# Kernel optimization log

Hardware: AMD Instinct MI355X
Metric: run time of the kernel (lower is better)

The kernel has to match this reference:

```python
import jax, jax.numpy as jnp
import numpy as np
import math

DIM = 1024
H = 16
DK = DIM // H
SEG = 512
NN = 2      # num_neighbors
DIL = 4     # dilation
B, L = 2, 8192


def setup_inputs() -> dict:
    key = jax.random.key(0)
    ks = jax.random.split(key, 9)
    scale = 1.0 / math.sqrt(DIM)
    def lin(k):
        return jax.random.normal(k, (DIM, DIM), jnp.float32) * scale
    return {
        "x": jax.random.normal(ks[0], (B, L, DIM), jnp.float32),
        "Wq": lin(ks[1]), "bq": jnp.zeros((DIM,), jnp.float32),
        "Wk": lin(ks[2]), "bk": jnp.zeros((DIM,), jnp.float32),
        "Wv": lin(ks[3]), "bv": jnp.zeros((DIM,), jnp.float32),
        "Wo": lin(ks[4]), "bo": jnp.zeros((DIM,), jnp.float32),
    }


def _attn(q, k, v):
    # q: [B,S,H,Q,dk], k/v: [B,S,H,K,dk]
    scores = jnp.einsum('bshqd,bshkd->bshqk', q, k) / math.sqrt(q.shape[-1])
    a = jax.nn.softmax(scores, axis=-1)
    return jnp.einsum('bshqk,bshkd->bshqd', a, v)


def reference(x, Wq, bq, Wk, bk, Wv, bv, Wo, bo):
    Bx, Lx, C = x.shape
    pad = (-Lx) % SEG

    def proj_chunk(W, b):
        t = x @ W + b                                  # [B,L,C]
        t = jnp.pad(t, ((0, 0), (0, pad), (0, 0)))
        S = t.shape[1] // SEG
        t = t.reshape(Bx, S, SEG, H, DK)
        return t.transpose(0, 1, 3, 2, 4)              # [B,S,H,seg,dk]

    q = proj_chunk(Wq, bq)
    k = proj_chunk(Wk, bk)
    v = proj_chunk(Wv, bv)
    S = q.shape[1]

    # segment-local dense attention (vectorized over all segments)
    out = _attn(q, k, v)

    # dilated sampling of neighbor segments' keys/values
    dil_idx = jnp.arange(0, SEG, DIL)
    kd = k[:, :, :, dil_idx, :]                        # [B,S,H,seg/DIL,dk]
    vd = v[:, :, :, dil_idx, :]

    seg_ids = jnp.arange(S)
    w = 1.0 / (2 * NN)
    for off in range(1, NN + 1):
        for sign in (-1, 1):
            n = seg_ids + sign * off
            valid = (n >= 0) & (n < S)                 # [S]
            nc = jnp.clip(n, 0, S - 1)
            cross = _attn(q, kd[:, nc], vd[:, nc])     # [B,S,H,seg,dk]
            out = out + jnp.where(valid[None, :, None, None, None], cross * w, 0.0)

    out = out.transpose(0, 1, 3, 2, 4).reshape(Bx, S * SEG, C)
    out = out[:, :Lx, :]
    return out @ Wo + bo
```

## Files before the change

### kernel.cpp

```cpp
#include <hip/hip_runtime.h>
#include <stdint.h>

typedef __attribute__((ext_vector_type(8))) short short8;
typedef __attribute__((ext_vector_type(4))) float f32x4;

#define MFMA16(A_, B_, C_) __builtin_amdgcn_mfma_f32_16x16x32_bf16((A_), (B_), (C_), 0, 0, 0)

#if __has_builtin(__builtin_amdgcn_exp2f)
#define EXP2(x) __builtin_amdgcn_exp2f(x)
#else
#define EXP2(x) exp2f(x)
#endif

#define GLDS16(g_, l_)                                                        \
  __builtin_amdgcn_global_load_lds(                                           \
      (const __attribute__((address_space(1))) void*)(g_),                    \
      (__attribute__((address_space(3))) void*)(l_), 16, 0, 0)

__device__ __forceinline__ unsigned short f2bf(float f) {
  unsigned int u = __float_as_uint(f);
  u += 0x7fffu + ((u >> 16) & 1u);
  return (unsigned short)(u >> 16);
}

__device__ __forceinline__ unsigned pk2(float a, float b) {
  return (__float_as_uint(a) >> 16) | (__float_as_uint(b) & 0xffff0000u);
}


__global__ void cast_x_kernel(const float* __restrict__ x,
                              unsigned short* __restrict__ xb, int n8) {
  int i = blockIdx.x * blockDim.x + threadIdx.x;
  if (i >= n8) return;
  const float4* x4 = reinterpret_cast<const float4*>(x);
  float4 a = x4[2 * i], b = x4[2 * i + 1];
  uint4 o;
  o.x = (unsigned)f2bf(a.x) | ((unsigned)f2bf(a.y) << 16);
  o.y = (unsigned)f2bf(a.z) | ((unsigned)f2bf(a.w) << 16);
  o.z = (unsigned)f2bf(b.x) | ((unsigned)f2bf(b.y) << 16);
  o.w = (unsigned)f2bf(b.z) | ((unsigned)f2bf(b.w) << 16);
  reinterpret_cast<uint4*>(xb)[i] = o;
}

__global__ void transpose_cast4_kernel(const float* __restrict__ W0,
                                       const float* __restrict__ W1,
                                       const float* __restrict__ W2,
                                       const float* __restrict__ W3,
                                       unsigned short* __restrict__ T0,
                                       unsigned short* __restrict__ T1,
                                       unsigned short* __restrict__ T2,
                                       unsigned short* __restrict__ T3) {
  __shared__ float tile[32][33];
  const float* W = (blockIdx.z == 0) ? W0 : (blockIdx.z == 1) ? W1
                   : (blockIdx.z == 2) ? W2 : W3;
  unsigned short* Wt = (blockIdx.z == 0) ? T0 : (blockIdx.z == 1) ? T1
                       : (blockIdx.z == 2) ? T2 : T3;
  int k0 = blockIdx.x * 32, n0 = blockIdx.y * 32;
  int tx = threadIdx.x, ty = threadIdx.y;
  for (int i = ty; i < 32; i += 8)
    tile[i][tx] = W[(size_t)(k0 + i) * 1024 + n0 + tx];
  __syncthreads();
  for (int i = ty; i < 32; i += 8)
    Wt[(size_t)(n0 + i) * 1024 + k0 + tx] = f2bf(tile[tx][i]);
}

template<int MODE>
__global__ __launch_bounds__(256, 2) void gemm_kernel(
    const unsigned short* __restrict__ A,
    const unsigned short* __restrict__ W,
    const float* __restrict__ bias,
    unsigned short* __restrict__ out_bf,
    unsigned short* __restrict__ out_vtd,
    float* __restrict__ out_f) {
  __shared__ unsigned short Asm[2][128 * 64];
  __shared__ unsigned short Bsm[2][128 * 64];
  const int t = threadIdx.x;
  const int wg = (blockIdx.x & 7) * 128 + (blockIdx.x >> 3);
  const int m0 = (wg >> 3) * 128;
  const int n0 = (wg & 7) * 128;
  const int w = t >> 6, lane = t & 63, lr = lane & 15, lg = lane >> 4;
  const int wm = w >> 1, wn = w & 1;

  f32x4 acc[4][4];
#pragma unroll
  for (int i = 0; i < 4; ++i)
#pragma unroll
    for (int j = 0; j < 4; ++j) acc[i][j] = f32x4{0.f, 0.f, 0.f, 0.f};

  const int srow = lane >> 3;
  const int sswz = ((lane & 7) ^ srow) * 8;
  const int mrow = m0 + w * 32 + srow;
  const unsigned short* gA;
  size_t astep, arstride;
  if (MODE == 3) {
    gA = A + (size_t)(mrow >> 9) * (16 * 32768) + (size_t)(mrow & 511) * 64 + sswz;
    astep = 32768;
    arstride = 8 * 64;
  } else {
    gA = A + (size_t)mrow * 1024 + sswz;
    astep = 64;
    arstride = 8 * 1024;
  }
  const unsigned short* gB = W + (size_t)(n0 + w * 32 + srow) * 1024 + sswz;

  auto stage = [&](int buf, int kt) {
    const unsigned short* ga = gA + (size_t)kt * astep;
    const unsigned short* gb = gB + (size_t)kt * 64;
    unsigned short* la = &Asm[buf][(w * 32) * 64];
    unsigned short* lb = &Bsm[buf][(w * 32) * 64];
#pragma unroll
    for (int p = 0; p < 4; ++p) {
      GLDS16(ga + (size_t)p * arstride, la + p * 8 * 64);
      GLDS16(gb + (size_t)(p * 8) * 1024, lb + p * 8 * 64);
    }
  };

  const int rswz = (lr & 7);
  auto compute = [&](int buf) {
    const unsigned short* bA = &Asm[buf][0];
    const unsigned short* bB = &Bsm[buf][0];
    short8 bfv[2][4];
#pragma unroll
    for (int ks = 0; ks < 2; ++ks)
#pragma unroll
      for (int j = 0; j < 4; ++j) {
        const int row = wn * 64 + j * 16 + lr;
        bfv[ks][j] = *reinterpret_cast<const short8*>(
            &bB[row * 64 + (((ks * 4 + lg) ^ rswz) * 8)]);
      }
#pragma unroll
    for (int i = 0; i < 4; ++i) {
      const int row = wm * 64 + i * 16 + lr;
      short8 af[2];
#pragma unroll
      for (int ks = 0; ks < 2; ++ks)
        af[ks] = *reinterpret_cast<const short8*>(
            &bA[row * 64 + (((ks * 4 + lg) ^ rswz) * 8)]);
#pragma unroll
      for (int ks = 0; ks < 2; ++ks)
#pragma unroll
        for (int j = 0; j < 4; ++j)
          acc[i][j] = MFMA16(af[ks], bfv[ks][j], acc[i][j]);
    }
  };

  stage(0, 0);
#pragma unroll 1
  for (int kt = 0; kt < 15; ++kt) {
    stage((kt + 1) & 1, kt + 1);
    asm volatile("s_waitcnt vmcnt(8)\n\ts_barrier" ::: "memory");
    compute(kt & 1);
    asm volatile("s_waitcnt lgkmcnt(0)\n\ts_barrier" ::: "memory");
  }
  asm volatile("s_waitcnt vmcnt(0)\n\ts_barrier" ::: "memory");
  compute(1);

#pragma unroll
  for (int i = 0; i < 4; ++i)
#pragma unroll
    for (int j = 0; j < 4; ++j) {
      const int n = n0 + wn * 64 + j * 16 + lr;
      const float bv = bias[n];
#pragma unroll
      for (int r = 0; r < 4; ++r) {
        const int m = m0 + wm * 64 + i * 16 + lg * 4 + r;
        float val = acc[i][j][r] + bv;
        if (MODE == 3) {
          out_f[(size_t)m * 1024 + n] = val;
        } else {
          const int b = m >> 13, ll = m & 8191;
          const int ss = ll >> 9, rr = ll & 511;
          const int hh = n >> 6, d = n & 63;
          const size_t head = (size_t)((b * 16 + ss) * 16 + hh);
          if (MODE == 0) {
            out_bf[head * 32768 + rr * 64 + d] = f2bf(val * 0.18033688011112042f);
          } else if (MODE == 1) {
            out_bf[head * 32768 + rr * 64 + d] = f2bf(val);
          } else {
            const int p32 = (((rr >> 2) & 3) << 3) | (((rr >> 4) & 1) << 2) | (rr & 3);
            out_bf[head * 32768 + (size_t)d * 512 + ((rr & ~31) | p32)] = f2bf(val);
            if ((rr & 3) == 0) {
              const int cd = rr >> 2;
              const int pd = (((cd >> 2) & 3) << 3) | (((cd >> 4) & 1) << 2) | (cd & 3);
              out_vtd[head * 8192 + (size_t)d * 128 + ((cd & ~31) | pd)] = f2bf(val);
            }
          }
        }
      }
    }
}

__device__ __forceinline__ void attn_group(
    const unsigned short* __restrict__ Kp, int kstride,
    const unsigned short* __restrict__ Vp, int vstride,
    int nchunks, float wgt,
    const short8 (&qf)[2][2],
    unsigned short* __restrict__ Kl, unsigned short* __restrict__ Vl,
    f32x4 (&total)[2][4],
    int lr, int lg, int w, int lane) {
  const int srow = lane >> 3;
  const int fcw = (lane & 7) ^ srow;
  const unsigned short* gK = Kp + (size_t)(w * 8 + srow) * kstride + fcw * 8;
  const unsigned short* gV = Vp + (size_t)(w * 8 + srow) * vstride + fcw * 8;
  const int sx = lr & 7;

  float l[2][2] = {{0.f, 0.f}, {0.f, 0.f}};
  f32x4 acc[2][4];
#pragma unroll
  for (int rt = 0; rt < 2; ++rt)
#pragma unroll
    for (int dt = 0; dt < 4; ++dt) acc[rt][dt] = f32x4{0.f, 0.f, 0.f, 0.f};

  GLDS16(gK, Kl + w * 512);
  GLDS16(gV, Vl + w * 512);
  __syncthreads();

  int cur = 0;
  for (int c = 0; c < nchunks; ++c) {
    if (c + 1 < nchunks) {
      GLDS16(gK + (size_t)((c + 1) * 64) * kstride, Kl + (cur ^ 1) * 4096 + w * 512);
      GLDS16(gV + (c + 1) * 64, Vl + (cur ^ 1) * 4096 + w * 512);
    }
    const unsigned short* bK = Kl + cur * 4096;
    const unsigned short* bV = Vl + cur * 4096;

    short8 pf[2][2];
#pragma unroll
    for (int kp = 0; kp < 2; ++kp) {
      f32x4 s0[2], s1[2];
#pragma unroll
      for (int rt = 0; rt < 2; ++rt) {
        s0[rt] = f32x4{0.f, 0.f, 0.f, 0.f};
        s1[rt] = f32x4{0.f, 0.f, 0.f, 0.f};
      }
      __builtin_amdgcn_s_setprio(1);
#pragma unroll
      for (int ks = 0; ks < 2; ++ks) {
        const int rc = (((ks * 4 + lg) ^ sx) * 8);
        short8 kf0 = *reinterpret_cast<const short8*>(&bK[(kp * 32 + lr) * 64 + rc]);
        short8 kf1 = *reinterpret_cast<const short8*>(&bK[(kp * 32 + 16 + lr) * 64 + rc]);
#pragma unroll
        for (int rt = 0; rt < 2; ++rt) {
          s0[rt] = MFMA16(kf0, qf[rt][ks], s0[rt]);
          s1[rt] = MFMA16(kf1, qf[rt][ks], s1[rt]);
        }
      }
      __builtin_amdgcn_s_setprio(0);
#pragma unroll
      for (int rt = 0; rt < 2; ++rt) {
        float e0 = EXP2(s0[rt][0]), e1 = EXP2(s0[rt][1]);
        float e2 = EXP2(s0[rt][2]), e3 = EXP2(s0[rt][3]);
        float e4 = EXP2(s1[rt][0]), e5 = EXP2(s1[rt][1]);
        float e6 = EXP2(s1[rt][2]), e7 = EXP2(s1[rt][3]);
        l[rt][kp] += ((e0 + e1) + (e2 + e3)) + ((e4 + e5) + (e6 + e7));
        uint4 wv;
        wv.x = pk2(e0, e1); wv.y = pk2(e2, e3);
        wv.z = pk2(e4, e5); wv.w = pk2(e6, e7);
        pf[rt][kp] = *reinterpret_cast<short8*>(&wv);
      }
    }
    __builtin_amdgcn_s_setprio(1);
#pragma unroll
    for (int ks = 0; ks < 2; ++ks) {
      const int rcv = (((ks * 4 + lg) ^ sx) * 8);
#pragma unroll
      for (int dt = 0; dt < 4; ++dt) {
        short8 vf = *reinterpret_cast<const short8*>(&bV[(dt * 16 + lr) * 64 + rcv]);
#pragma unroll
        for (int rt = 0; rt < 2; ++rt)
          acc[rt][dt] = MFMA16(pf[rt][ks], vf, acc[rt][dt]);
      }
    }
    __builtin_amdgcn_s_setprio(0);
    __syncthreads();
    cur ^= 1;
  }
#pragma unroll
  for (int rt = 0; rt < 2; ++rt) {
    float s = l[rt][0] + l[rt][1];
    s += __shfl_xor(s, 16);
    s += __shfl_xor(s, 32);
    float rl[4];
#pragma unroll
    for (int r = 0; r < 4; ++r) rl[r] = wgt / __shfl(s, lg * 4 + r);
#pragma unroll
    for (int dt = 0; dt < 4; ++dt)
#pragma unroll
      for (int r = 0; r < 4; ++r) total[rt][dt][r] += acc[rt][dt][r] * rl[r];
  }
}

__global__ __launch_bounds__(512) void attn_kernel(
    const unsigned short* __restrict__ Q,
    const unsigned short* __restrict__ K,
    const unsigned short* __restrict__ Vt,
    const unsigned short* __restrict__ Vtd,
    unsigned short* __restrict__ AO) {
  __shared__ unsigned short Kl[2 * 4096];
  __shared__ unsigned short Vl[2 * 4096];
  const int wg = blockIdx.x;
  const int qh = wg & 1;
  const int bsh = wg >> 1;
  const int h = bsh & 15, s = (bsh >> 4) & 15, b = bsh >> 8;
  const int t = threadIdx.x, w = t >> 6, lane = t & 63, lr = lane & 15, lg = lane >> 4;
  const int q0 = qh * 256 + w * 32;

  const size_t headbase = (size_t)((b * 16 + s) * 16 + h);
  const unsigned short* Qp = Q + headbase * 32768 + (size_t)q0 * 64;
  short8 qf[2][2];
#pragma unroll
  for (int rt = 0; rt < 2; ++rt)
#pragma unroll
    for (int ks = 0; ks < 2; ++ks)
      qf[rt][ks] = *reinterpret_cast<const short8*>(&Qp[(rt * 16 + lr) * 64 + ks * 32 + lg * 8]);

  f32x4 total[2][4];
#pragma unroll
  for (int rt = 0; rt < 2; ++rt)
#pragma unroll
    for (int dt = 0; dt < 4; ++dt) total[rt][dt] = f32x4{0.f, 0.f, 0.f, 0.f};

  attn_group(K + headbase * 32768, 64, Vt + headbase * 32768, 512, 8, 1.0f,
             qf, Kl, Vl, total, lr, lg, w, lane);
#pragma unroll
  for (int gi = 0; gi < 4; ++gi) {
    const int off = (gi == 0) ? -2 : (gi == 1) ? -1 : (gi == 2) ? 1 : 2;
    const int ns = s + off;
    if (ns < 0 || ns > 15) continue;
    const size_t hb = (size_t)((b * 16 + ns) * 16 + h);
    attn_group(K + hb * 32768, 256, Vtd + hb * 8192, 128, 2, 0.25f,
               qf, Kl, Vl, total, lr, lg, w, lane);
  }
  const size_t obase = headbase * 32768 + (size_t)q0 * 64;
#pragma unroll
  for (int rt = 0; rt < 2; ++rt)
#pragma unroll
    for (int dt = 0; dt < 4; ++dt)
#pragma unroll
      for (int r = 0; r < 4; ++r) {
        const int q = rt * 16 + lg * 4 + r;
        const int d = dt * 16 + lr;
        AO[obase + (size_t)q * 64 + d] = f2bf(total[rt][dt][r]);
      }
}

extern "C" void kernel_launch(void* const* d_in, const int* in_sizes, int n_in,
                              void* d_out, int out_size, void* d_ws, size_t ws_size,
                              hipStream_t stream) {
  const float* x  = (const float*)d_in[0];
  const float* Wq = (const float*)d_in[1];
  const float* bq = (const float*)d_in[2];
  const float* Wk = (const float*)d_in[3];
  const float* bk = (const float*)d_in[4];
  const float* Wv = (const float*)d_in[5];
  const float* bv = (const float*)d_in[6];
  const float* Wo = (const float*)d_in[7];
  const float* bo = (const float*)d_in[8];
  float* out = (float*)d_out;

  char* ws = (char*)d_ws;
  unsigned short* Xb   = (unsigned short*)(ws);
  unsigned short* Wqt  = (unsigned short*)(ws + 33554432);
  unsigned short* Wkt  = (unsigned short*)(ws + 35651584);
  unsigned short* Wvt  = (unsigned short*)(ws + 37748736);
  unsigned short* Wot  = (unsigned short*)(ws + 39845888);
  unsigned short* Qb   = (unsigned short*)(ws + 41943040);
  unsigned short* Kb   = (unsigned short*)(ws + 75497472);
  unsigned short* Vtb  = (unsigned short*)(ws + 109051904);
  unsigned short* Vtdb = (unsigned short*)(ws + 142606336);
  unsigned short* AOb  = (unsigned short*)(ws + 150994944);

  cast_x_kernel<<<8192, 256, 0, stream>>>(x, Xb, 2097152);
  dim3 tb(32, 8), tg(32, 32, 4);
  transpose_cast4_kernel<<<tg, tb, 0, stream>>>(Wq, Wk, Wv, Wo, Wqt, Wkt, Wvt, Wot);

  gemm_kernel<0><<<1024, 256, 0, stream>>>(Xb, Wqt, bq, Qb, nullptr, nullptr);
  gemm_kernel<1><<<1024, 256, 0, stream>>>(Xb, Wkt, bk, Kb, nullptr, nullptr);
  gemm_kernel<2><<<1024, 256, 0, stream>>>(Xb, Wvt, bv, Vtb, Vtdb, nullptr);

  attn_kernel<<<1024, 512, 0, stream>>>(Qb, Kb, Vtb, Vtdb, AOb);

  gemm_kernel<3><<<1024, 256, 0, stream>>>(AOb, Wot, bo, nullptr, nullptr, out);
}
```

Baseline: 292.1 us.

## Enlarge GEMM tiles to 256x256 with 32x32 MFMA and remap attention blocks

The projection and output GEMMs move from 128x128 tiles with 4 waves to 256x256 tiles with 8 waves per block. They now use 32x32x16 bf16 MFMA instructions in place of 16x16x32, with the fragment indexing and epilogue row mapping updated to match. The grid shrinks to 256 blocks, about one per CU, which is meant to raise operand reuse and cut LDS reads per MFMA. The cost is 128KB of LDS per block and a single wave of blocks that may leave little latency hiding. The attention kernel's block index is also reordered so the two query halves of a head land in different halves of the grid.

```diff
diff --git a/kernel.cpp b/kernel.cpp
--- a/kernel.cpp
+++ b/kernel.cpp
@@ -3,8 +3,10 @@
 
 typedef __attribute__((ext_vector_type(8))) short short8;
 typedef __attribute__((ext_vector_type(4))) float f32x4;
+typedef __attribute__((ext_vector_type(16))) float f32x16;
 
 #define MFMA16(A_, B_, C_) __builtin_amdgcn_mfma_f32_16x16x32_bf16((A_), (B_), (C_), 0, 0, 0)
+#define MFMA32(A_, B_, C_) __builtin_amdgcn_mfma_f32_32x32x16_bf16((A_), (B_), (C_), 0, 0, 0)
 
 #if __has_builtin(__builtin_amdgcn_exp2f)
 #define EXP2(x) __builtin_amdgcn_exp2f(x)
@@ -65,27 +67,30 @@
 }
 
 template<int MODE>
-__global__ __launch_bounds__(256, 2) void gemm_kernel(
+__global__ __launch_bounds__(512, 2) void gemm_kernel(
     const unsigned short* __restrict__ A,
     const unsigned short* __restrict__ W,
     const float* __restrict__ bias,
     unsigned short* __restrict__ out_bf,
     unsigned short* __restrict__ out_vtd,
     float* __restrict__ out_f) {
-  __shared__ unsigned short Asm[2][128 * 64];
-  __shared__ unsigned short Bsm[2][128 * 64];
+  __shared__ unsigned short Asm[2][256 * 64];
+  __shared__ unsigned short Bsm[2][256 * 64];
   const int t = threadIdx.x;
-  const int wg = (blockIdx.x & 7) * 128 + (blockIdx.x >> 3);
-  const int m0 = (wg >> 3) * 128;
-  const int n0 = (wg & 7) * 128;
-  const int w = t >> 6, lane = t & 63, lr = lane & 15, lg = lane >> 4;
-  const int wm = w >> 1, wn = w & 1;
-
-  f32x4 acc[4][4];
+  const int wg = (blockIdx.x & 7) * 32 + (blockIdx.x >> 3);
+  const int m0 = (wg >> 2) * 256;
+  const int n0 = (wg & 3) * 256;
+  const int w = t >> 6, lane = t & 63;
+  const int wm = w >> 2, wn = w & 3;
+  const int rl = lane & 31, l5 = lane >> 5;
+
+  f32x16 acc[4][2];
 #pragma unroll
   for (int i = 0; i < 4; ++i)
 #pragma unroll
-    for (int j = 0; j < 4; ++j) acc[i][j] = f32x4{0.f, 0.f, 0.f, 0.f};
+    for (int j = 0; j < 2; ++j)
+#pragma unroll
+      for (int e = 0; e < 16; ++e) acc[i][j][e] = 0.f;
 
   const int srow = lane >> 3;
   const int sswz = ((lane & 7) ^ srow) * 8;
@@ -115,32 +120,32 @@
     }
   };
 
-  const int rswz = (lr & 7);
+  const int rswz = (rl & 7);
   auto compute = [&](int buf) {
     const unsigned short* bA = &Asm[buf][0];
     const unsigned short* bB = &Bsm[buf][0];
-    short8 bfv[2][4];
-#pragma unroll
-    for (int ks = 0; ks < 2; ++ks)
-#pragma unroll
-      for (int j = 0; j < 4; ++j) {
-        const int row = wn * 64 + j * 16 + lr;
+    short8 bfv[4][2];
+#pragma unroll
+    for (int ks = 0; ks < 4; ++ks)
+#pragma unroll
+      for (int j = 0; j < 2; ++j) {
+        const int row = wn * 64 + j * 32 + rl;
         bfv[ks][j] = *reinterpret_cast<const short8*>(
-            &bB[row * 64 + (((ks * 4 + lg) ^ rswz) * 8)]);
+            &bB[row * 64 + (((ks * 2 + l5) ^ rswz) * 8)]);
       }
 #pragma unroll
     for (int i = 0; i < 4; ++i) {
-      const int row = wm * 64 + i * 16 + lr;
-      short8 af[2];
-#pragma unroll
-      for (int ks = 0; ks < 2; ++ks)
+      const int row = wm * 128 + i * 32 + rl;
+      short8 af[4];
+#pragma unroll
+      for (int ks = 0; ks < 4; ++ks)
         af[ks] = *reinterpret_cast<const short8*>(
-            &bA[row * 64 + (((ks * 4 + lg) ^ rswz) * 8)]);
-#pragma unroll
-      for (int ks = 0; ks < 2; ++ks)
-#pragma unroll
-        for (int j = 0; j < 4; ++j)
-          acc[i][j] = MFMA16(af[ks], bfv[ks][j], acc[i][j]);
+            &bA[row * 64 + (((ks * 2 + l5) ^ rswz) * 8)]);
+#pragma unroll
+      for (int ks = 0; ks < 4; ++ks)
+#pragma unroll
+        for (int j = 0; j < 2; ++j)
+          acc[i][j] = MFMA32(af[ks], bfv[ks][j], acc[i][j]);
     }
   };
 
@@ -158,13 +163,13 @@
 #pragma unroll
   for (int i = 0; i < 4; ++i)
 #pragma unroll
-    for (int j = 0; j < 4; ++j) {
-      const int n = n0 + wn * 64 + j * 16 + lr;
+    for (int j = 0; j < 2; ++j) {
+      const int n = n0 + wn * 64 + j * 32 + rl;
       const float bv = bias[n];
 #pragma unroll
-      for (int r = 0; r < 4; ++r) {
-        const int m = m0 + wm * 64 + i * 16 + lg * 4 + r;
-        float val = acc[i][j][r] + bv;
+      for (int reg = 0; reg < 16; ++reg) {
+        const int m = m0 + wm * 128 + i * 32 + (reg & 3) + 8 * (reg >> 2) + 4 * l5;
+        float val = acc[i][j][reg] + bv;
         if (MODE == 3) {
           out_f[(size_t)m * 1024 + n] = val;
         } else {
@@ -299,8 +304,8 @@
   __shared__ unsigned short Kl[2 * 4096];
   __shared__ unsigned short Vl[2 * 4096];
   const int wg = blockIdx.x;
-  const int qh = wg & 1;
-  const int bsh = wg >> 1;
+  const int qh = wg >> 9;
+  const int bsh = wg & 511;
   const int h = bsh & 15, s = (bsh >> 4) & 15, b = bsh >> 8;
   const int t = threadIdx.x, w = t >> 6, lane = t & 63, lr = lane & 15, lg = lane >> 4;
   const int q0 = qh * 256 + w * 32;
@@ -374,11 +379,11 @@
   dim3 tb(32, 8), tg(32, 32, 4);
   transpose_cast4_kernel<<<tg, tb, 0, stream>>>(Wq, Wk, Wv, Wo, Wqt, Wkt, Wvt, Wot);
 
-  gemm_kernel<0><<<1024, 256, 0, stream>>>(Xb, Wqt, bq, Qb, nullptr, nullptr);
-  gemm_kernel<1><<<1024, 256, 0, stream>>>(Xb, Wkt, bk, Kb, nullptr, nullptr);
-  gemm_kernel<2><<<1024, 256, 0, stream>>>(Xb, Wvt, bv, Vtb, Vtdb, nullptr);
+  gemm_kernel<0><<<256, 512, 0, stream>>>(Xb, Wqt, bq, Qb, nullptr, nullptr);
+  gemm_kernel<1><<<256, 512, 0, stream>>>(Xb, Wkt, bk, Kb, nullptr, nullptr);
+  gemm_kernel<2><<<256, 512, 0, stream>>>(Xb, Wvt, bv, Vtb, Vtdb, nullptr);
 
   attn_kernel<<<1024, 512, 0, stream>>>(Qb, Kb, Vtb, Vtdb, AOb);
 
-  gemm_kernel<3><<<1024, 256, 0, stream>>>(AOb, Wot, bo, nullptr, nullptr, out);
-}
+  gemm_kernel<3><<<256, 512, 0, stream>>>(AOb, Wot, bo, nullptr, nullptr, out);
+}
```

New measurement: 306.2 us. +4.8%, slower.
